# Performance work log

Measured on AMD Instinct MI355X. Metric: run time of the kernel, lower is better.

The kernel has to match this reference:

```python
import jax, jax.numpy as jnp
import numpy as np

EMBED_SIZE = 1024
HEADS = 16
HEAD_DIM = EMBED_SIZE // HEADS
N, L = 2, 2048


def setup_inputs() -> dict:
    key = jax.random.key(0)
    ks = jax.random.split(key, 6)
    values = jax.random.normal(ks[0], (N, L, EMBED_SIZE), dtype=jnp.float32)
    keys_t = jax.random.normal(ks[1], (N, L, EMBED_SIZE), dtype=jnp.float32)
    query = jax.random.normal(ks[2], (N, L, EMBED_SIZE), dtype=jnp.float32)
    mask = jax.random.randint(ks[3], (N, 1, L, L), 0, 2, dtype=jnp.int32)
    # fc_out params (torch Linear: y = x @ W.T + b)
    Wo = jax.random.normal(ks[4], (EMBED_SIZE, EMBED_SIZE), dtype=jnp.float32) * (EMBED_SIZE ** -0.5)
    bo = jax.random.normal(ks[5], (EMBED_SIZE,), dtype=jnp.float32) * 0.01
    return {"values": values, "keys": keys_t, "query": query, "mask": mask, "Wo": Wo, "bo": bo}


def reference(values, keys, query, mask, Wo, bo):
    # NOTE: the original torch module defines per-head q/k/v Linears but never
    # calls them in forward; only fc_out is applied. We reproduce that exactly.
    n, q_len, _ = query.shape
    v = values.reshape(n, -1, HEADS, HEAD_DIM)   # nkhd
    k = keys.reshape(n, -1, HEADS, HEAD_DIM)     # nkhd
    q = query.reshape(n, q_len, HEADS, HEAD_DIM) # nqhd
    energy = jnp.einsum('nqhd,nkhd->nhqk', q, k)
    energy = jnp.where(mask == 0, jnp.float32(-1e20), energy)
    scale = jnp.float32(EMBED_SIZE) ** 0.5  # sqrt(embed_size), as in source
    attn = jax.nn.softmax(energy / scale, axis=3)
    out = jnp.einsum('nhqk,nkhd->nqhd', attn, v).reshape(n, q_len, HEADS * HEAD_DIM)
    return out @ Wo.T + bo
```

## Files before the change

kernel.cpp:

```cpp
#include <hip/hip_runtime.h>
#include <hip/hip_bf16.h>
#include <stdint.h>

#define LSEQ 2048
#define NBATCH 2
#define NHEADS 16
#define HDIM 64
#define EMB 1024

typedef __bf16 bf16x8 __attribute__((ext_vector_type(8)));
typedef float f32x4 __attribute__((ext_vector_type(4)));
typedef unsigned short ushort4v __attribute__((ext_vector_type(4)));
typedef unsigned short ushort8v __attribute__((ext_vector_type(8)));

#define QSCALE (1.44269504088896f / 32.0f)

static __device__ __forceinline__ unsigned short f2bf(float f) {
  union { float f; uint32_t u; } v; v.f = f;
  uint32_t u = v.u;
  u += 0x7fffu + ((u >> 16) & 1u);
  return (unsigned short)(u >> 16);
}

static __device__ __forceinline__ f32x4 mfma16(bf16x8 a, bf16x8 b, f32x4 c) {
  return __builtin_amdgcn_mfma_f32_16x16x32_bf16(a, b, c, 0, 0, 0);
}

static __device__ __forceinline__ float mexp2(float e, uint32_t m, int b) {
  uint32_t keep = (uint32_t)__builtin_amdgcn_sbfe((int)m, b, 1);
  return __uint_as_float(__float_as_uint(__builtin_amdgcn_exp2f(e)) & keep);
}

__global__ __launch_bounds__(256) void prep_kernel(
    const float* __restrict__ q, const float* __restrict__ k,
    const float* __restrict__ w, const int* __restrict__ mask,
    const float* __restrict__ v,
    unsigned short* __restrict__ qb, unsigned short* __restrict__ kb,
    unsigned short* __restrict__ wb, unsigned char* __restrict__ mb8,
    unsigned short* __restrict__ vt) {
  int b = blockIdx.x;
  if (b < 8192) {
    int idx = b * 256 + threadIdx.x;
    const float* src; unsigned short* dst; int t; int swz;
    if (idx < (1 << 20)) { src = q; dst = qb; t = idx; swz = 0; }
    else                 { src = k; dst = kb; t = idx - (1 << 20); swz = 1; }
    int e = t << 2;
    int d = e & 63;
    int h = (e >> 6) & 15;
    int l = (e >> 10) & (LSEQ - 1);
    int n = e >> 21;
    float4 vv = reinterpret_cast<const float4*>(src)[t];
    int dd = d;
    if (swz) dd = ((((d >> 3) ^ (l & 7)) << 3) | (d & 7));
    else { vv.x *= QSCALE; vv.y *= QSCALE; vv.z *= QSCALE; vv.w *= QSCALE; }
    ushort4v o;
    o.x = f2bf(vv.x); o.y = f2bf(vv.y); o.z = f2bf(vv.z); o.w = f2bf(vv.w);
    size_t oi = (((size_t)n * NHEADS + h) * LSEQ + l) * HDIM + dd;
    *reinterpret_cast<ushort4v*>(dst + oi) = o;
  } else if (b < 9216) {
    int t = (b - 8192) * 256 + threadIdx.x;
    float4 vv = reinterpret_cast<const float4*>(w)[t];
    ushort4v o;
    o.x = f2bf(vv.x); o.y = f2bf(vv.y); o.z = f2bf(vv.z); o.w = f2bf(vv.w);
    reinterpret_cast<ushort4v*>(wb)[t] = o;
  } else if (b < 13312) {
    int idx = (b - 9216) * 256 + threadIdx.x;
    const int* mp = mask + (size_t)idx * 8;
    int4 m0 = *reinterpret_cast<const int4*>(mp);
    int4 m1 = *reinterpret_cast<const int4*>(mp + 4);
    unsigned int bb = (m0.x ? 1u : 0u) | (m0.y ? 2u : 0u) | (m0.z ? 4u : 0u) |
                      (m0.w ? 8u : 0u) | (m1.x ? 16u : 0u) | (m1.y ? 32u : 0u) |
                      (m1.z ? 64u : 0u) | (m1.w ? 128u : 0u);
    mb8[idx] = (unsigned char)bb;
  } else {
    int b2 = b - 13312;
    int kc = b2 & 63;
    int h  = (b2 >> 6) & 15;
    int n  = b2 >> 10;
    int t  = threadIdx.x;
    int d    = t & 63;
    int sgrp = t >> 6;
    const float* src = v + (size_t)n * LSEQ * EMB + h * HDIM + d;
    ushort8v o;
#pragma unroll
    for (int j = 0; j < 8; ++j) {
      int kp = (j < 4) ? (4 * sgrp + j) : (16 + 4 * sgrp + (j - 4));
      float f = src[(size_t)(kc * 32 + kp) * EMB];
      o[j] = f2bf(f);
    }
    int cs = sgrp ^ ((d >> 1) & 3);
    size_t base = (((size_t)(n * NHEADS + h) * 64 + kc) * HDIM + d) * 32 + (cs << 3);
    *reinterpret_cast<ushort8v*>(vt + base) = o;
  }
}

__global__ __launch_bounds__(512, 4) void attn_kernel(
    const unsigned short* __restrict__ Kb, const unsigned short* __restrict__ Qb,
    const unsigned short* __restrict__ VT, const uint32_t* __restrict__ maskw,
    unsigned short* __restrict__ Op) {
  __shared__ unsigned short lds[2][16384];

  int bid = blockIdx.x;
  bid = (bid & 7) * 64 + (bid >> 3);
  int qt = bid & 15;
  int h  = (bid >> 4) & 15;
  int n  = bid >> 8;
  int tid  = threadIdx.x;
  int wave = tid >> 6;
  int lane = tid & 63;
  int g  = lane >> 4;
  int qi = lane & 15;
  int qrow = qt * 128 + wave * 16 + qi;

  const unsigned short* qptr = Qb + (((size_t)n * NHEADS + h) * LSEQ + qrow) * HDIM;
  bf16x8 bq0 = *reinterpret_cast<const bf16x8*>(qptr + g * 8);
  bf16x8 bq1 = *reinterpret_cast<const bf16x8*>(qptr + 32 + g * 8);

  const unsigned short* khead  = Kb + (((size_t)n * NHEADS + h) * LSEQ) * HDIM;
  const unsigned short* vthead = VT + ((size_t)(n * NHEADS + h) * 64) * (HDIM * 32);
  const uint32_t* mrow = maskw + ((size_t)n * LSEQ + qrow) * 64;

  int xk = qi & 7;
  int kA = qi * 64 + ((g ^ xk) << 3);
  int kB = qi * 64 + (((4 + g) ^ xk) << 3);
  int kC = kA + 1024;
  int kD = kB + 1024;
  int xv = (qi >> 1) & 3;
  int vA = qi * 32 + ((g ^ xv) << 3);

  union { uint32_t u[4]; bf16x8 v; } ones;
  ones.u[0] = 0x3F803F80u; ones.u[1] = 0x3F803F80u;
  ones.u[2] = 0x3F803F80u; ones.u[3] = 0x3F803F80u;

  f32x4 z = {0.f, 0.f, 0.f, 0.f};
  f32x4 acc0 = z, acc1 = z, acc2 = z, acc3 = z;
  f32x4 sacc = z;

#define STAGE(T, BUF) do {                                                     \
    const unsigned short* kg_ = khead  + (size_t)(T) * 8192 + tid * 8;         \
    const unsigned short* vg_ = vthead + (size_t)(T) * 8192 + tid * 8;         \
    _Pragma("unroll")                                                          \
    for (int j_ = 0; j_ < 2; ++j_) {                                           \
      __builtin_amdgcn_global_load_lds(                                        \
          (const __attribute__((address_space(1))) uint32_t*)(kg_ + j_ * 4096),\
          (__attribute__((address_space(3))) uint32_t*)                        \
              &lds[BUF][j_ * 4096 + wave * 512],                               \
          16, 0, 0);                                                           \
      __builtin_amdgcn_global_load_lds(                                        \
          (const __attribute__((address_space(1))) uint32_t*)(vg_ + j_ * 4096),\
          (__attribute__((address_space(3))) uint32_t*)                        \
              &lds[BUF][8192 + j_ * 4096 + wave * 512],                        \
          16, 0, 0);                                                           \
    }                                                                          \
  } while (0)

#define COMPUTE(BUF, CH, MW) do {                                              \
    const unsigned short* lk_ = &lds[BUF][(CH) * 2048];                        \
    const unsigned short* lv_ = &lds[BUF][8192 + (CH) * 2048];                 \
    bf16x8 K0 = *(const bf16x8*)(lk_ + kA);                                    \
    bf16x8 K1 = *(const bf16x8*)(lk_ + kB);                                    \
    bf16x8 K2 = *(const bf16x8*)(lk_ + kC);                                    \
    bf16x8 K3 = *(const bf16x8*)(lk_ + kD);                                    \
    f32x4 e0 = z, e1 = z;                                                      \
    e0 = mfma16(K0, bq0, e0); e0 = mfma16(K1, bq1, e0);                        \
    e1 = mfma16(K2, bq0, e1); e1 = mfma16(K3, bq1, e1);                        \
    bf16x8 V0 = *(const bf16x8*)(lv_ + vA);                                    \
    bf16x8 V1 = *(const bf16x8*)(lv_ + vA + 512);                              \
    bf16x8 V2 = *(const bf16x8*)(lv_ + vA + 1024);                             \
    bf16x8 V3 = *(const bf16x8*)(lv_ + vA + 1536);                             \
    uint32_t m0_ = (MW) >> (4 * g);                                            \
    uint32_t m1_ = (MW) >> (16 + 4 * g);                                       \
    float p0 = mexp2(e0[0], m0_, 0);                                           \
    float p1 = mexp2(e0[1], m0_, 1);                                           \
    float p2 = mexp2(e0[2], m0_, 2);                                           \
    float p3 = mexp2(e0[3], m0_, 3);                                           \
    float p4 = mexp2(e1[0], m1_, 0);                                           \
    float p5 = mexp2(e1[1], m1_, 1);                                           \
    float p6 = mexp2(e1[2], m1_, 2);                                           \
    float p7 = mexp2(e1[3], m1_, 3);                                           \
    union { uint32_t u[4]; bf16x8 v; } pf;                                     \
    asm("v_cvt_pk_bf16_f32 %0, %1, %2" : "=v"(pf.u[0]) : "v"(p0), "v"(p1));    \
    asm("v_cvt_pk_bf16_f32 %0, %1, %2" : "=v"(pf.u[1]) : "v"(p2), "v"(p3));    \
    asm("v_cvt_pk_bf16_f32 %0, %1, %2" : "=v"(pf.u[2]) : "v"(p4), "v"(p5));    \
    asm("v_cvt_pk_bf16_f32 %0, %1, %2" : "=v"(pf.u[3]) : "v"(p6), "v"(p7));    \
    acc0 = mfma16(V0, pf.v, acc0);                                             \
    acc1 = mfma16(V1, pf.v, acc1);                                             \
    acc2 = mfma16(V2, pf.v, acc2);                                             \
    acc3 = mfma16(V3, pf.v, acc3);                                             \
    sacc = mfma16(ones.v, pf.v, sacc);                                         \
  } while (0)

  uint4 mw0 = *(const uint4*)(mrow);
  uint4 mw1, mw2;
  STAGE(0, 0);
  __syncthreads();

  for (int t = 0; t < 16; t += 2) {
    int t1 = (t + 1) & 15;
    mw1 = *(const uint4*)(mrow + 4 * t1);
    STAGE(t1, 1);
    __builtin_amdgcn_s_setprio(1);
    COMPUTE(0, 0, mw0.x);
    COMPUTE(0, 1, mw0.y);
    COMPUTE(0, 2, mw0.z);
    COMPUTE(0, 3, mw0.w);
    __builtin_amdgcn_s_setprio(0);
    __syncthreads();
    int t2 = (t + 2) & 15;
    mw2 = *(const uint4*)(mrow + 4 * t2);
    STAGE(t2, 0);
    __builtin_amdgcn_s_setprio(1);
    COMPUTE(1, 0, mw1.x);
    COMPUTE(1, 1, mw1.y);
    COMPUTE(1, 2, mw1.z);
    COMPUTE(1, 3, mw1.w);
    __builtin_amdgcn_s_setprio(0);
    __syncthreads();
    mw0 = mw2;
  }
#undef STAGE
#undef COMPUTE

  float inv = 1.0f / sacc[0];

  size_t ob = ((size_t)n * LSEQ + qrow) * EMB + h * HDIM;
  ushort4v s0, s1, s2, s3;
#pragma unroll
  for (int r = 0; r < 4; ++r) {
    s0[r] = f2bf(acc0[r] * inv);
    s1[r] = f2bf(acc1[r] * inv);
    s2[r] = f2bf(acc2[r] * inv);
    s3[r] = f2bf(acc3[r] * inv);
  }
  *reinterpret_cast<ushort4v*>(Op + ob + 0  + 4 * g) = s0;
  *reinterpret_cast<ushort4v*>(Op + ob + 16 + 4 * g) = s1;
  *reinterpret_cast<ushort4v*>(Op + ob + 32 + 4 * g) = s2;
  *reinterpret_cast<ushort4v*>(Op + ob + 48 + 4 * g) = s3;
}

__global__ __launch_bounds__(256, 2) void proj_kernel(
    const unsigned short* __restrict__ A, const unsigned short* __restrict__ B,
    const float* __restrict__ bo, float* __restrict__ out) {
  __shared__ unsigned short plds[2][12288];

  int bid = blockIdx.x;
  bid = (bid & 7) * 64 + (bid >> 3);
  int mb0 = (bid >> 4) * 128;
  int nb0 = (bid & 15) * 64;
  int tid  = threadIdx.x;
  int wave = tid >> 6;
  int lane = tid & 63;
  int g  = lane >> 4;
  int qi = lane & 15;
  int wm = wave >> 1, wn = wave & 1;

  int srow = tid >> 2;
  int scol = (((tid & 3) ^ ((tid >> 3) & 3)) << 3);
  const unsigned short* aS0 = A + (size_t)(mb0 + srow) * EMB + scol;
  const unsigned short* aS1 = aS0 + (size_t)64 * EMB;
  const unsigned short* bS  = B + (size_t)(nb0 + srow) * EMB + scol;

  int xa = (qi >> 1) & 3;
  int gof = ((g ^ xa) << 3);
  int aof0 = (wm * 64 + qi) * 32 + gof;
  int aof1 = aof0 + 16 * 32;
  int aof2 = aof0 + 32 * 32;
  int aof3 = aof0 + 48 * 32;
  int bof0 = (wn * 32 + qi) * 32 + gof;
  int bof1 = bof0 + 16 * 32;

  f32x4 z = {0.f, 0.f, 0.f, 0.f};
  f32x4 acc00 = z, acc01 = z, acc10 = z, acc11 = z;
  f32x4 acc20 = z, acc21 = z, acc30 = z, acc31 = z;

#define PSTAGE2(KT, BUF) do {                                                  \
    _Pragma("unroll")                                                          \
    for (int p_ = 0; p_ < 2; ++p_) {                                           \
      int kt_ = ((KT) + p_) & 31;                                              \
      __builtin_amdgcn_global_load_lds(                                        \
          (const __attribute__((address_space(1))) uint32_t*)(aS0 + kt_ * 32), \
          (__attribute__((address_space(3))) uint32_t*)                        \
              &plds[BUF][p_ * 6144 + wave * 512],                              \
          16, 0, 0);                                                           \
      __builtin_amdgcn_global_load_lds(                                        \
          (const __attribute__((address_space(1))) uint32_t*)(aS1 + kt_ * 32), \
          (__attribute__((address_space(3))) uint32_t*)                        \
              &plds[BUF][p_ * 6144 + 2048 + wave * 512],                       \
          16, 0, 0);                                                           \
      __builtin_amdgcn_global_load_lds(                                        \
          (const __attribute__((address_space(1))) uint32_t*)(bS + kt_ * 32),  \
          (__attribute__((address_space(3))) uint32_t*)                        \
              &plds[BUF][p_ * 6144 + 4096 + wave * 512],                       \
          16, 0, 0);                                                           \
    }                                                                          \
  } while (0)

#define PCOMPUTE(BUF, P) do {                                                  \
    const unsigned short* la_ = &plds[BUF][(P) * 6144];                        \
    const unsigned short* lb_ = &plds[BUF][(P) * 6144 + 4096];                 \
    bf16x8 a0 = *(const bf16x8*)(la_ + aof0);                                  \
    bf16x8 a1 = *(const bf16x8*)(la_ + aof1);                                  \
    bf16x8 a2 = *(const bf16x8*)(la_ + aof2);                                  \
    bf16x8 a3 = *(const bf16x8*)(la_ + aof3);                                  \
    bf16x8 b0 = *(const bf16x8*)(lb_ + bof0);                                  \
    bf16x8 b1 = *(const bf16x8*)(lb_ + bof1);                                  \
    acc00 = mfma16(a0, b0, acc00); acc01 = mfma16(a0, b1, acc01);              \
    acc10 = mfma16(a1, b0, acc10); acc11 = mfma16(a1, b1, acc11);              \
    acc20 = mfma16(a2, b0, acc20); acc21 = mfma16(a2, b1, acc21);              \
    acc30 = mfma16(a3, b0, acc30); acc31 = mfma16(a3, b1, acc31);              \
  } while (0)

  PSTAGE2(0, 0);
  __syncthreads();
  for (int kt = 0; kt < 32; kt += 4) {
    PSTAGE2(kt + 2, 1);
    PCOMPUTE(0, 0);
    PCOMPUTE(0, 1);
    __syncthreads();
    PSTAGE2((kt + 4) & 31, 0);
    PCOMPUTE(1, 0);
    PCOMPUTE(1, 1);
    __syncthreads();
  }
#undef PSTAGE2
#undef PCOMPUTE

  int orow = mb0 + wm * 64 + 4 * g;
  int col0 = nb0 + wn * 32 + qi;
  float bia0 = bo[col0];
  float bia1 = bo[col0 + 16];
#define PSTORE(ACC0, ACC1, M) do {                                             \
    _Pragma("unroll")                                                          \
    for (int r = 0; r < 4; ++r) {                                              \
      size_t rw = (size_t)(orow + (M) * 16 + r) * EMB;                         \
      out[rw + col0]      = ACC0[r] + bia0;                                    \
      out[rw + col0 + 16] = ACC1[r] + bia1;                                    \
    }                                                                          \
  } while (0)
  PSTORE(acc00, acc01, 0);
  PSTORE(acc10, acc11, 1);
  PSTORE(acc20, acc21, 2);
  PSTORE(acc30, acc31, 3);
#undef PSTORE
}

extern "C" void kernel_launch(void* const* d_in, const int* in_sizes, int n_in,
                              void* d_out, int out_size, void* d_ws, size_t ws_size,
                              hipStream_t stream) {
  const float* Vf   = (const float*)d_in[0];
  const float* Kf   = (const float*)d_in[1];
  const float* Qf   = (const float*)d_in[2];
  const int*   Mask = (const int*)d_in[3];
  const float* Wo   = (const float*)d_in[4];
  const float* Bo   = (const float*)d_in[5];
  float* out = (float*)d_out;

  char* ws = (char*)d_ws;
  unsigned short* Qb  = (unsigned short*)(ws);
  unsigned short* Kb  = (unsigned short*)(ws + (size_t)8  * 1024 * 1024);
  unsigned short* VTb = (unsigned short*)(ws + (size_t)16 * 1024 * 1024);
  unsigned short* Wob = (unsigned short*)(ws + (size_t)24 * 1024 * 1024);
  unsigned short* Opb = (unsigned short*)(ws + (size_t)26 * 1024 * 1024);
  unsigned char*  Mb  = (unsigned char*)(ws + (size_t)34 * 1024 * 1024);

  prep_kernel<<<15360, 256, 0, stream>>>(Qf, Kf, Wo, Mask, Vf, Qb, Kb, Wob, Mb, VTb);
  attn_kernel<<<512, 512, 0, stream>>>(Kb, Qb, VTb, (const uint32_t*)Mb, Opb);
  proj_kernel<<<512, 256, 0, stream>>>(Opb, Wob, Bo, out);
}
```

Measured before the change: 82.69 us.

## Switch attention kernel to 32x32x16 MFMA tiles with 4 waves per block

Rewrites the attention inner loop to use 32x32x16 bf16 MFMA instead of 16x16x32. Each wave now covers 32 query rows, so a block runs 4 waves of 256 threads instead of 8. The V-transpose layout and swizzle in prep are changed to match, and permlane32_swap reorders the probability fragments for the PV product. The goal is fewer MFMA issues and LDS reads per FLOP, at the cost of more registers per wave, fewer waves per block to hide latency, and dropping the s_setprio hints.

```diff
diff --git a/kernel.cpp b/kernel.cpp
--- a/kernel.cpp
+++ b/kernel.cpp
@@ -10,6 +10,7 @@
 
 typedef __bf16 bf16x8 __attribute__((ext_vector_type(8)));
 typedef float f32x4 __attribute__((ext_vector_type(4)));
+typedef float f32x16 __attribute__((ext_vector_type(16)));
 typedef unsigned short ushort4v __attribute__((ext_vector_type(4)));
 typedef unsigned short ushort8v __attribute__((ext_vector_type(8)));
 
@@ -25,11 +26,19 @@
 static __device__ __forceinline__ f32x4 mfma16(bf16x8 a, bf16x8 b, f32x4 c) {
   return __builtin_amdgcn_mfma_f32_16x16x32_bf16(a, b, c, 0, 0, 0);
 }
+static __device__ __forceinline__ f32x16 mfma32(bf16x8 a, bf16x8 b, f32x16 c) {
+  return __builtin_amdgcn_mfma_f32_32x32x16_bf16(a, b, c, 0, 0, 0);
+}
 
 static __device__ __forceinline__ float mexp2(float e, uint32_t m, int b) {
   uint32_t keep = (uint32_t)__builtin_amdgcn_sbfe((int)m, b, 1);
   return __uint_as_float(__float_as_uint(__builtin_amdgcn_exp2f(e)) & keep);
 }
+
+#define PLSWAP(X, Y) do {                                                      \
+    auto rr_ = __builtin_amdgcn_permlane32_swap((X), (Y), false, false);       \
+    (X) = rr_[0]; (Y) = rr_[1];                                                \
+  } while (0)
 
 __global__ __launch_bounds__(256) void prep_kernel(
     const float* __restrict__ q, const float* __restrict__ k,
@@ -84,17 +93,16 @@
     ushort8v o;
 #pragma unroll
     for (int j = 0; j < 8; ++j) {
-      int kp = (j < 4) ? (4 * sgrp + j) : (16 + 4 * sgrp + (j - 4));
-      float f = src[(size_t)(kc * 32 + kp) * EMB];
+      float f = src[(size_t)(kc * 32 + sgrp * 8 + j) * EMB];
       o[j] = f2bf(f);
     }
-    int cs = sgrp ^ ((d >> 1) & 3);
+    int cs = sgrp ^ (d & 3);
     size_t base = (((size_t)(n * NHEADS + h) * 64 + kc) * HDIM + d) * 32 + (cs << 3);
     *reinterpret_cast<ushort8v*>(vt + base) = o;
   }
 }
 
-__global__ __launch_bounds__(512, 4) void attn_kernel(
+__global__ __launch_bounds__(256, 2) void attn_kernel(
     const unsigned short* __restrict__ Kb, const unsigned short* __restrict__ Qb,
     const unsigned short* __restrict__ VT, const uint32_t* __restrict__ maskw,
     unsigned short* __restrict__ Op) {
@@ -108,48 +116,53 @@
   int tid  = threadIdx.x;
   int wave = tid >> 6;
   int lane = tid & 63;
-  int g  = lane >> 4;
-  int qi = lane & 15;
-  int qrow = qt * 128 + wave * 16 + qi;
+  int hi = lane >> 5;
+  int lq = lane & 31;
+  int qrow = qt * 128 + wave * 32 + lq;
 
   const unsigned short* qptr = Qb + (((size_t)n * NHEADS + h) * LSEQ + qrow) * HDIM;
-  bf16x8 bq0 = *reinterpret_cast<const bf16x8*>(qptr + g * 8);
-  bf16x8 bq1 = *reinterpret_cast<const bf16x8*>(qptr + 32 + g * 8);
+  bf16x8 q0 = *reinterpret_cast<const bf16x8*>(qptr + 0  + 8 * hi);
+  bf16x8 q1 = *reinterpret_cast<const bf16x8*>(qptr + 16 + 8 * hi);
+  bf16x8 q2 = *reinterpret_cast<const bf16x8*>(qptr + 32 + 8 * hi);
+  bf16x8 q3 = *reinterpret_cast<const bf16x8*>(qptr + 48 + 8 * hi);
 
   const unsigned short* khead  = Kb + (((size_t)n * NHEADS + h) * LSEQ) * HDIM;
   const unsigned short* vthead = VT + ((size_t)(n * NHEADS + h) * 64) * (HDIM * 32);
   const uint32_t* mrow = maskw + ((size_t)n * LSEQ + qrow) * 64;
 
-  int xk = qi & 7;
-  int kA = qi * 64 + ((g ^ xk) << 3);
-  int kB = qi * 64 + (((4 + g) ^ xk) << 3);
-  int kC = kA + 1024;
-  int kD = kB + 1024;
-  int xv = (qi >> 1) & 3;
-  int vA = qi * 32 + ((g ^ xv) << 3);
+  int kO0 = lq * 64 + (((0 + hi) ^ (lq & 7)) << 3);
+  int kO1 = lq * 64 + (((2 + hi) ^ (lq & 7)) << 3);
+  int kO2 = lq * 64 + (((4 + hi) ^ (lq & 7)) << 3);
+  int kO3 = lq * 64 + (((6 + hi) ^ (lq & 7)) << 3);
+  int vO00 = (lq) * 32      + (((0 + hi) ^ (lq & 3)) << 3);
+  int vO01 = (lq) * 32      + (((2 + hi) ^ (lq & 3)) << 3);
+  int vO10 = (32 + lq) * 32 + (((0 + hi) ^ (lq & 3)) << 3);
+  int vO11 = (32 + lq) * 32 + (((2 + hi) ^ (lq & 3)) << 3);
+  int hi4 = 4 * hi;
 
   union { uint32_t u[4]; bf16x8 v; } ones;
   ones.u[0] = 0x3F803F80u; ones.u[1] = 0x3F803F80u;
   ones.u[2] = 0x3F803F80u; ones.u[3] = 0x3F803F80u;
 
-  f32x4 z = {0.f, 0.f, 0.f, 0.f};
-  f32x4 acc0 = z, acc1 = z, acc2 = z, acc3 = z;
-  f32x4 sacc = z;
+  const f32x16 z16 = {0.f,0.f,0.f,0.f,0.f,0.f,0.f,0.f,
+                      0.f,0.f,0.f,0.f,0.f,0.f,0.f,0.f};
+  f32x16 acc0 = z16, acc1 = z16;
+  f32x16 sacc = z16;
 
 #define STAGE(T, BUF) do {                                                     \
     const unsigned short* kg_ = khead  + (size_t)(T) * 8192 + tid * 8;         \
     const unsigned short* vg_ = vthead + (size_t)(T) * 8192 + tid * 8;         \
     _Pragma("unroll")                                                          \
-    for (int j_ = 0; j_ < 2; ++j_) {                                           \
-      __builtin_amdgcn_global_load_lds(                                        \
-          (const __attribute__((address_space(1))) uint32_t*)(kg_ + j_ * 4096),\
-          (__attribute__((address_space(3))) uint32_t*)                        \
-              &lds[BUF][j_ * 4096 + wave * 512],                               \
-          16, 0, 0);                                                           \
-      __builtin_amdgcn_global_load_lds(                                        \
-          (const __attribute__((address_space(1))) uint32_t*)(vg_ + j_ * 4096),\
-          (__attribute__((address_space(3))) uint32_t*)                        \
-              &lds[BUF][8192 + j_ * 4096 + wave * 512],                        \
+    for (int j_ = 0; j_ < 4; ++j_) {                                           \
+      __builtin_amdgcn_global_load_lds(                                        \
+          (const __attribute__((address_space(1))) uint32_t*)(kg_ + j_ * 2048),\
+          (__attribute__((address_space(3))) uint32_t*)                        \
+              &lds[BUF][j_ * 2048 + wave * 512],                               \
+          16, 0, 0);                                                           \
+      __builtin_amdgcn_global_load_lds(                                        \
+          (const __attribute__((address_space(1))) uint32_t*)(vg_ + j_ * 2048),\
+          (__attribute__((address_space(3))) uint32_t*)                        \
+              &lds[BUF][8192 + j_ * 2048 + wave * 512],                        \
           16, 0, 0);                                                           \
     }                                                                          \
   } while (0)
@@ -157,37 +170,42 @@
 #define COMPUTE(BUF, CH, MW) do {                                              \
     const unsigned short* lk_ = &lds[BUF][(CH) * 2048];                        \
     const unsigned short* lv_ = &lds[BUF][8192 + (CH) * 2048];                 \
-    bf16x8 K0 = *(const bf16x8*)(lk_ + kA);                                    \
-    bf16x8 K1 = *(const bf16x8*)(lk_ + kB);                                    \
-    bf16x8 K2 = *(const bf16x8*)(lk_ + kC);                                    \
-    bf16x8 K3 = *(const bf16x8*)(lk_ + kD);                                    \
-    f32x4 e0 = z, e1 = z;                                                      \
-    e0 = mfma16(K0, bq0, e0); e0 = mfma16(K1, bq1, e0);                        \
-    e1 = mfma16(K2, bq0, e1); e1 = mfma16(K3, bq1, e1);                        \
-    bf16x8 V0 = *(const bf16x8*)(lv_ + vA);                                    \
-    bf16x8 V1 = *(const bf16x8*)(lv_ + vA + 512);                              \
-    bf16x8 V2 = *(const bf16x8*)(lv_ + vA + 1024);                             \
-    bf16x8 V3 = *(const bf16x8*)(lv_ + vA + 1536);                             \
-    uint32_t m0_ = (MW) >> (4 * g);                                            \
-    uint32_t m1_ = (MW) >> (16 + 4 * g);                                       \
-    float p0 = mexp2(e0[0], m0_, 0);                                           \
-    float p1 = mexp2(e0[1], m0_, 1);                                           \
-    float p2 = mexp2(e0[2], m0_, 2);                                           \
-    float p3 = mexp2(e0[3], m0_, 3);                                           \
-    float p4 = mexp2(e1[0], m1_, 0);                                           \
-    float p5 = mexp2(e1[1], m1_, 1);                                           \
-    float p6 = mexp2(e1[2], m1_, 2);                                           \
-    float p7 = mexp2(e1[3], m1_, 3);                                           \
-    union { uint32_t u[4]; bf16x8 v; } pf;                                     \
-    asm("v_cvt_pk_bf16_f32 %0, %1, %2" : "=v"(pf.u[0]) : "v"(p0), "v"(p1));    \
-    asm("v_cvt_pk_bf16_f32 %0, %1, %2" : "=v"(pf.u[1]) : "v"(p2), "v"(p3));    \
-    asm("v_cvt_pk_bf16_f32 %0, %1, %2" : "=v"(pf.u[2]) : "v"(p4), "v"(p5));    \
-    asm("v_cvt_pk_bf16_f32 %0, %1, %2" : "=v"(pf.u[3]) : "v"(p6), "v"(p7));    \
-    acc0 = mfma16(V0, pf.v, acc0);                                             \
-    acc1 = mfma16(V1, pf.v, acc1);                                             \
-    acc2 = mfma16(V2, pf.v, acc2);                                             \
-    acc3 = mfma16(V3, pf.v, acc3);                                             \
-    sacc = mfma16(ones.v, pf.v, sacc);                                         \
+    bf16x8 K0 = *(const bf16x8*)(lk_ + kO0);                                   \
+    bf16x8 K1 = *(const bf16x8*)(lk_ + kO1);                                   \
+    bf16x8 K2 = *(const bf16x8*)(lk_ + kO2);                                   \
+    bf16x8 K3 = *(const bf16x8*)(lk_ + kO3);                                   \
+    f32x16 e = z16;                                                            \
+    e = mfma32(K0, q0, e); e = mfma32(K1, q1, e);                              \
+    e = mfma32(K2, q2, e); e = mfma32(K3, q3, e);                              \
+    uint32_t mh_ = (MW) >> hi4;                                                \
+    float p[16];                                                               \
+    _Pragma("unroll")                                                          \
+    for (int r_ = 0; r_ < 16; ++r_)                                            \
+      p[r_] = mexp2(e[r_], mh_, (r_ & 3) + 8 * (r_ >> 2));                     \
+    uint32_t a0_, a1_, a2_, a3_, b0_, b1_, b2_, b3_;                           \
+    asm("v_cvt_pk_bf16_f32 %0, %1, %2" : "=v"(a0_) : "v"(p[0]),  "v"(p[1]));   \
+    asm("v_cvt_pk_bf16_f32 %0, %1, %2" : "=v"(a1_) : "v"(p[2]),  "v"(p[3]));   \
+    asm("v_cvt_pk_bf16_f32 %0, %1, %2" : "=v"(a2_) : "v"(p[4]),  "v"(p[5]));   \
+    asm("v_cvt_pk_bf16_f32 %0, %1, %2" : "=v"(a3_) : "v"(p[6]),  "v"(p[7]));   \
+    asm("v_cvt_pk_bf16_f32 %0, %1, %2" : "=v"(b0_) : "v"(p[8]),  "v"(p[9]));   \
+    asm("v_cvt_pk_bf16_f32 %0, %1, %2" : "=v"(b1_) : "v"(p[10]), "v"(p[11]));  \
+    asm("v_cvt_pk_bf16_f32 %0, %1, %2" : "=v"(b2_) : "v"(p[12]), "v"(p[13]));  \
+    asm("v_cvt_pk_bf16_f32 %0, %1, %2" : "=v"(b3_) : "v"(p[14]), "v"(p[15]));  \
+    PLSWAP(a0_, a2_); PLSWAP(a1_, a3_);                                        \
+    PLSWAP(b0_, b2_); PLSWAP(b1_, b3_);                                        \
+    union { uint32_t u[4]; bf16x8 v; } pf0, pf1;                               \
+    pf0.u[0] = a0_; pf0.u[1] = a1_; pf0.u[2] = a2_; pf0.u[3] = a3_;            \
+    pf1.u[0] = b0_; pf1.u[1] = b1_; pf1.u[2] = b2_; pf1.u[3] = b3_;            \
+    bf16x8 V00 = *(const bf16x8*)(lv_ + vO00);                                 \
+    bf16x8 V01 = *(const bf16x8*)(lv_ + vO01);                                 \
+    bf16x8 V10 = *(const bf16x8*)(lv_ + vO10);                                 \
+    bf16x8 V11 = *(const bf16x8*)(lv_ + vO11);                                 \
+    acc0 = mfma32(V00, pf0.v, acc0);                                           \
+    acc0 = mfma32(V01, pf1.v, acc0);                                           \
+    acc1 = mfma32(V10, pf0.v, acc1);                                           \
+    acc1 = mfma32(V11, pf1.v, acc1);                                           \
+    sacc = mfma32(ones.v, pf0.v, sacc);                                        \
+    sacc = mfma32(ones.v, pf1.v, sacc);                                        \
   } while (0)
 
   uint4 mw0 = *(const uint4*)(mrow);
@@ -199,22 +217,18 @@
     int t1 = (t + 1) & 15;
     mw1 = *(const uint4*)(mrow + 4 * t1);
     STAGE(t1, 1);
-    __builtin_amdgcn_s_setprio(1);
     COMPUTE(0, 0, mw0.x);
     COMPUTE(0, 1, mw0.y);
     COMPUTE(0, 2, mw0.z);
     COMPUTE(0, 3, mw0.w);
-    __builtin_amdgcn_s_setprio(0);
     __syncthreads();
     int t2 = (t + 2) & 15;
     mw2 = *(const uint4*)(mrow + 4 * t2);
     STAGE(t2, 0);
-    __builtin_amdgcn_s_setprio(1);
     COMPUTE(1, 0, mw1.x);
     COMPUTE(1, 1, mw1.y);
     COMPUTE(1, 2, mw1.z);
     COMPUTE(1, 3, mw1.w);
-    __builtin_amdgcn_s_setprio(0);
     __syncthreads();
     mw0 = mw2;
   }
@@ -224,18 +238,17 @@
   float inv = 1.0f / sacc[0];
 
   size_t ob = ((size_t)n * LSEQ + qrow) * EMB + h * HDIM;
-  ushort4v s0, s1, s2, s3;
 #pragma unroll
-  for (int r = 0; r < 4; ++r) {
-    s0[r] = f2bf(acc0[r] * inv);
-    s1[r] = f2bf(acc1[r] * inv);
-    s2[r] = f2bf(acc2[r] * inv);
-    s3[r] = f2bf(acc3[r] * inv);
+  for (int rq = 0; rq < 4; ++rq) {
+    ushort4v s0, s1;
+#pragma unroll
+    for (int j = 0; j < 4; ++j) {
+      s0[j] = f2bf(acc0[rq * 4 + j] * inv);
+      s1[j] = f2bf(acc1[rq * 4 + j] * inv);
+    }
+    *reinterpret_cast<ushort4v*>(Op + ob + 4 * hi + 8 * rq) = s0;
+    *reinterpret_cast<ushort4v*>(Op + ob + 32 + 4 * hi + 8 * rq) = s1;
   }
-  *reinterpret_cast<ushort4v*>(Op + ob + 0  + 4 * g) = s0;
-  *reinterpret_cast<ushort4v*>(Op + ob + 16 + 4 * g) = s1;
-  *reinterpret_cast<ushort4v*>(Op + ob + 32 + 4 * g) = s2;
-  *reinterpret_cast<ushort4v*>(Op + ob + 48 + 4 * g) = s3;
 }
 
 __global__ __launch_bounds__(256, 2) void proj_kernel(
@@ -364,6 +377,6 @@
   unsigned char*  Mb  = (unsigned char*)(ws + (size_t)34 * 1024 * 1024);
 
   prep_kernel<<<15360, 256, 0, stream>>>(Qf, Kf, Wo, Mask, Vf, Qb, Kb, Wob, Mb, VTb);
-  attn_kernel<<<512, 512, 0, stream>>>(Kb, Qb, VTb, (const uint32_t*)Mb, Opb);
+  attn_kernel<<<512, 256, 0, stream>>>(Kb, Qb, VTb, (const uint32_t*)Mb, Opb);
   proj_kernel<<<512, 256, 0, stream>>>(Opb, Wob, Bo, out);
 }
```

New measurement: 88.55 us. 1.07x slower.
